# Optimization experiments

Hardware: AMD Instinct MI355X
Metric: run time of the kernel (lower is better)

The kernel has to match this reference:

```python
import jax, jax.numpy as jnp
import numpy as np

B, N, D = 4, 4096, 128
H = 128  # hidden_size == input_size (required by residual add)

def setup_inputs() -> dict:
    key = jax.random.key(0)
    kx, kw, kb = jax.random.split(key, 3)
    x = jax.random.normal(kx, (B, N, D), dtype=jnp.float32)
    # nn.Linear(input_size, hidden_size): weight [H, D], bias [H]
    lim = 1.0 / np.sqrt(D)
    W = jax.random.uniform(kw, (H, D), dtype=jnp.float32, minval=-lim, maxval=lim)
    b = jax.random.uniform(kb, (H,), dtype=jnp.float32, minval=-lim, maxval=lim)
    return {"x": x, "W": W, "b": b}

def reference(x, W, b):
    # adj[b,i,j] = <x[b,i], x[b,j]>, relu
    adj = jax.nn.relu(jnp.einsum('bid,bjd->bij', x, x))  # [B,N,N]
    # torch sums over dim=1 (rows) -> per-column sums, then divides columns
    col_sum = adj.sum(axis=1)                 # [B,N]
    adj = adj / col_sum[:, None, :]           # broadcast over dim 1
    out = jnp.einsum('bij,bjd->bid', adj, x)  # aggregate
    out = jnp.tanh(jnp.einsum('bnd,hd->bnh', out, W) + b)
    # Dropout(0.5) treated as eval-mode identity
    return out + x  # residual=True
```

## Files before the change

### kernel.cpp

```cpp
#include <hip/hip_runtime.h>
#include <hip/hip_bf16.h>

#define BN 4
#define NN 4096
#define DD 128

typedef __attribute__((ext_vector_type(8))) __bf16 bf16x8;
typedef __attribute__((ext_vector_type(4))) float f32x4;

typedef union {
  bf16x8 v;
  unsigned int u[4];
  uint2 u2[2];
} pk8;

typedef __attribute__((address_space(1))) const unsigned int* gas_p;
typedef __attribute__((address_space(3))) unsigned int* las_p;

__device__ __forceinline__ void gload16(const void* g, void* l) {
  __builtin_amdgcn_global_load_lds((gas_p)g, (las_p)l, 16, 0, 0);
}
__device__ __forceinline__ void wait_vm0() {
  asm volatile("s_waitcnt vmcnt(0)" ::: "memory");
}
__device__ __forceinline__ void wait_vm4() {
  asm volatile("s_waitcnt vmcnt(4)" ::: "memory");
}
__device__ __forceinline__ unsigned int cvtpk(float lo, float hi) {
  unsigned int r;
  asm("v_cvt_pk_bf16_f32 %0, %1, %2" : "=v"(r) : "v"(lo), "v"(hi));
  return r;
}
__device__ __forceinline__ unsigned int pkrelu(float lo, float hi) {
  return cvtpk(fmaxf(lo, 0.f), fmaxf(hi, 0.f));
}

__device__ inline unsigned short f2bf(float f) {
  unsigned int u = __float_as_uint(f);
  unsigned int r = (u + 0x7FFFu + ((u >> 16) & 1u)) >> 16;
  return (unsigned short)r;
}
__device__ inline float bf2f(unsigned short s) {
  return __uint_as_float(((unsigned int)s) << 16);
}

__global__ __launch_bounds__(256) void k_cvt(const float* __restrict__ x,
                                             unsigned short* __restrict__ xb) {
  int i = (blockIdx.x * 256 + threadIdx.x) * 8;
  float4 a = *(const float4*)(x + i);
  float4 c = *(const float4*)(x + i + 4);
  uint4 o;
  o.x = cvtpk(a.x, a.y);
  o.y = cvtpk(a.z, a.w);
  o.z = cvtpk(c.x, c.y);
  o.w = cvtpk(c.z, c.w);
  *(uint4*)(xb + i) = o;
}

__global__ __launch_bounds__(256, 4) void k_colsum(const unsigned short* __restrict__ xb,
                                                   float* __restrict__ colpart) {
  __shared__ unsigned short XiB[2][64 * 128];
  const int b = blockIdx.y, j0 = blockIdx.x * 128, ic = blockIdx.z;
  const int tid = threadIdx.x, lane = tid & 63, wv = tid >> 6;
  const unsigned short* xbb = xb + b * NN * DD;
  const int g = lane >> 4;
  const int ibeg = ic * (NN / 8);
  const int nt = (NN / 8) / 64;

#pragma unroll
  for (int hb = 0; hb < 2; ++hb)
#pragma unroll
    for (int q = 0; q < 4; ++q) {
      int c = wv * 4 + q;
      int lr = c * 4 + g;
      int gsrc = (lane & 15) ^ (lr & 7);
      gload16(&xbb[(j0 + hb * 64 + lr) * 128 + gsrc * 8], &XiB[hb][c * 512]);
    }
  wait_vm0();
  __syncthreads();

  bf16x8 bfr[2][4];
#pragma unroll
  for (int ni = 0; ni < 2; ++ni)
#pragma unroll
    for (int kk = 0; kk < 4; ++kk) {
      int lr = (wv & 1) * 32 + ni * 16 + (lane & 15);
      bfr[ni][kk] = *(const bf16x8*)&XiB[wv >> 1][lr * 128 + (((kk * 4 + g) ^ (lr & 7)) << 3)];
    }
  __syncthreads();

#pragma unroll
  for (int q = 0; q < 4; ++q) {
    int c = wv * 4 + q;
    int lr = c * 4 + g;
    int gsrc = (lane & 15) ^ (lr & 7);
    gload16(&xbb[(ibeg + lr) * 128 + gsrc * 8], &XiB[1][c * 512]);
  }

  int basek[4];
#pragma unroll
  for (int kk = 0; kk < 4; ++kk)
    basek[kk] = (lane & 15) * 128 + (((kk * 4 + g) ^ (lane & 7)) << 3);

  float colacc0 = 0.f, colacc1 = 0.f;
  for (int t = 0; t < nt; ++t) {
    wait_vm0();
    __syncthreads();
    const int cur = (t + 1) & 1, nxt = t & 1;
    if (t + 1 < nt) {
      const int i1 = ibeg + (t + 1) * 64;
#pragma unroll
      for (int q = 0; q < 4; ++q) {
        int c = wv * 4 + q;
        int lr = c * 4 + g;
        int gsrc = (lane & 15) ^ (lr & 7);
        gload16(&xbb[(i1 + lr) * 128 + gsrc * 8], &XiB[nxt][c * 512]);
      }
    }
    f32x4 a0[4], a1[4];
#pragma unroll
    for (int mj = 0; mj < 4; ++mj) { a0[mj] = (f32x4){}; a1[mj] = (f32x4){}; }
    __builtin_amdgcn_s_setprio(1);
#pragma unroll
    for (int kk = 0; kk < 4; ++kk) {
      bf16x8 ar0 = *(const bf16x8*)&XiB[cur][basek[kk]];
      bf16x8 ar1 = *(const bf16x8*)&XiB[cur][basek[kk] + 1 * 2048];
      bf16x8 ar2 = *(const bf16x8*)&XiB[cur][basek[kk] + 2 * 2048];
      bf16x8 ar3 = *(const bf16x8*)&XiB[cur][basek[kk] + 3 * 2048];
      a0[0] = __builtin_amdgcn_mfma_f32_16x16x32_bf16(ar0, bfr[0][kk], a0[0], 0, 0, 0);
      a1[0] = __builtin_amdgcn_mfma_f32_16x16x32_bf16(ar0, bfr[1][kk], a1[0], 0, 0, 0);
      a0[1] = __builtin_amdgcn_mfma_f32_16x16x32_bf16(ar1, bfr[0][kk], a0[1], 0, 0, 0);
      a1[1] = __builtin_amdgcn_mfma_f32_16x16x32_bf16(ar1, bfr[1][kk], a1[1], 0, 0, 0);
      a0[2] = __builtin_amdgcn_mfma_f32_16x16x32_bf16(ar2, bfr[0][kk], a0[2], 0, 0, 0);
      a1[2] = __builtin_amdgcn_mfma_f32_16x16x32_bf16(ar2, bfr[1][kk], a1[2], 0, 0, 0);
      a0[3] = __builtin_amdgcn_mfma_f32_16x16x32_bf16(ar3, bfr[0][kk], a0[3], 0, 0, 0);
      a1[3] = __builtin_amdgcn_mfma_f32_16x16x32_bf16(ar3, bfr[1][kk], a1[3], 0, 0, 0);
    }
    __builtin_amdgcn_s_setprio(0);
    {
      float s0 = 0.f, s1 = 0.f;
#pragma unroll
      for (int mj = 0; mj < 4; ++mj)
#pragma unroll
        for (int r = 0; r < 4; ++r) {
          s0 += fmaxf(a0[mj][r], 0.f);
          s1 += fmaxf(a1[mj][r], 0.f);
        }
      s0 += __shfl_xor(s0, 16); s0 += __shfl_xor(s0, 32);
      s1 += __shfl_xor(s1, 16); s1 += __shfl_xor(s1, 32);
      colacc0 += s0; colacc1 += s1;
    }
  }
  if (lane < 16) {
    colpart[(ic * BN + b) * NN + j0 + wv * 32 + lane] = colacc0;
    colpart[(ic * BN + b) * NN + j0 + wv * 32 + 16 + lane] = colacc1;
  }
}

__global__ __launch_bounds__(256) void k_ytrans(const float* __restrict__ x,
                                                const float* __restrict__ colpart,
                                                unsigned short* __restrict__ yt) {
  __shared__ unsigned short T[64 * 72];
  const int b = blockIdx.z, j0 = blockIdx.y * 64, d0 = blockIdx.x * 64;
  const int tid = threadIdx.x;
  int jr = tid >> 2, q0 = (tid & 3) * 16;
  float cs = 0.f;
#pragma unroll
  for (int ic = 0; ic < 8; ++ic) cs += colpart[(ic * BN + b) * NN + j0 + jr];
  float inv = 1.0f / cs;
  const float* xr = x + (size_t)(b * NN + j0 + jr) * DD + d0 + q0;
#pragma unroll
  for (int q = 0; q < 4; ++q) {
    float4 v = *(const float4*)(xr + q * 4);
    int dc = q0 + q * 4;
    T[jr * 72 + dc + 0] = f2bf(v.x * inv);
    T[jr * 72 + dc + 1] = f2bf(v.y * inv);
    T[jr * 72 + dc + 2] = f2bf(v.z * inv);
    T[jr * 72 + dc + 3] = f2bf(v.w * inv);
  }
  __syncthreads();
  for (int c = tid; c < 512; c += 256) {
    int dr = c >> 3, jg = c & 7;
    alignas(16) unsigned short tmp[8];
#pragma unroll
    for (int u = 0; u < 8; ++u) {
      int jj = (jg >> 2) * 32 + (jg & 3) * 4 + (u & 3) + (u >> 2) * 16;
      tmp[u] = T[jj * 72 + dr];
    }
    *(uint4*)&yt[(size_t)(b * DD + d0 + dr) * NN + j0 + jg * 8] = *(const uint4*)tmp;
  }
}

__global__ __launch_bounds__(256, 2) void k_pass2(const unsigned short* __restrict__ xb,
                                                  const unsigned short* __restrict__ yt,
                                                  unsigned short* __restrict__ opart,
                                                  int jc) {
  __shared__ unsigned short XjB[2][64 * 128];
  __shared__ unsigned short YsB[3][128 * 64];
  const int b = blockIdx.y, i0 = blockIdx.x * 128, zc = blockIdx.z;
  const int tid = threadIdx.x, lane = tid & 63, wv = tid >> 6;
  const unsigned short* xbb = xb + b * NN * DD;
  const unsigned short* ytb = yt + (size_t)b * DD * NN;
  const int g = lane >> 4, l15 = lane & 15;

  const int jspan = NN / jc;
  const int jbeg = zc * jspan;
  const int nt = jspan / 64;

#pragma unroll
  for (int hb = 0; hb < 2; ++hb)
#pragma unroll
    for (int q = 0; q < 4; ++q) {
      int c = wv * 4 + q;
      int lr = c * 4 + g;
      int gsrc = l15 ^ (lr & 7);
      gload16(&xbb[(i0 + hb * 64 + lr) * 128 + gsrc * 8], &XjB[hb][c * 512]);
    }
  wait_vm0();
  __syncthreads();

  bf16x8 bfr[2][4];
#pragma unroll
  for (int ni = 0; ni < 2; ++ni)
#pragma unroll
    for (int kk = 0; kk < 4; ++kk) {
      int lr = (wv & 1) * 32 + ni * 16 + l15;
      bfr[ni][kk] = *(const bf16x8*)&XjB[wv >> 1][lr * 128 + (((kk * 4 + g) ^ (lr & 7)) << 3)];
    }
  __syncthreads();

#pragma unroll
  for (int q = 0; q < 4; ++q) {
    int c = wv * 4 + q;
    int lr = c * 4 + g;
    int gsrc = l15 ^ (lr & 7);
    gload16(&xbb[(jbeg + lr) * 128 + gsrc * 8], &XjB[0][c * 512]);
  }
#pragma unroll
  for (int q = 0; q < 4; ++q) {
    int c = wv * 4 + q;
    int dr = c * 8 + (lane >> 3);
    int gsrc = (lane & 7) ^ (dr & 7);
    gload16(&ytb[(size_t)dr * NN + jbeg + gsrc * 8], &YsB[0][c * 512]);
  }
  if (1 < nt) {
#pragma unroll
    for (int q = 0; q < 4; ++q) {
      int c = wv * 4 + q;
      int dr = c * 8 + (lane >> 3);
      int gsrc = (lane & 7) ^ (dr & 7);
      gload16(&ytb[(size_t)dr * NN + jbeg + 64 + gsrc * 8], &YsB[1][c * 512]);
    }
  }

  int xjb[4];
#pragma unroll
  for (int kk = 0; kk < 4; ++kk)
    xjb[kk] = l15 * 128 + (((kk * 4 + g) ^ (l15 & 7)) << 3);
  int ysb[2];
#pragma unroll
  for (int c = 0; c < 2; ++c)
    ysb[c] = l15 * 64 + (((c * 4 + g) ^ (l15 & 7)) << 3);

  f32x4 oacc0[8], oacc1[8];
#pragma unroll
  for (int n = 0; n < 8; ++n) { oacc0[n] = (f32x4){}; oacc1[n] = (f32x4){}; }

  int ybuf = 0;
  for (int t = 0; t < nt; ++t) {
    if (t + 1 < nt) wait_vm4(); else wait_vm0();
    __syncthreads();
    if (t + 1 < nt) {
      const int j1 = jbeg + (t + 1) * 64;
#pragma unroll
      for (int q = 0; q < 4; ++q) {
        int c = wv * 4 + q;
        int lr = c * 4 + g;
        int gsrc = l15 ^ (lr & 7);
        gload16(&xbb[(j1 + lr) * 128 + gsrc * 8], &XjB[(t + 1) & 1][c * 512]);
      }
      if (t + 2 < nt) {
        const int j2 = jbeg + (t + 2) * 64;
        int nb = ybuf + 2; if (nb >= 3) nb -= 3;
#pragma unroll
        for (int q = 0; q < 4; ++q) {
          int c = wv * 4 + q;
          int dr = c * 8 + (lane >> 3);
          int gsrc = (lane & 7) ^ (dr & 7);
          gload16(&ytb[(size_t)dr * NN + j2 + gsrc * 8], &YsB[nb][c * 512]);
        }
      }
    }
    const unsigned short* Xj = XjB[t & 1];
    const unsigned short* Ys = YsB[ybuf];

    f32x4 s0[4], s1[4];
#pragma unroll
    for (int mj = 0; mj < 4; ++mj) { s0[mj] = (f32x4){}; s1[mj] = (f32x4){}; }
    __builtin_amdgcn_s_setprio(1);
#pragma unroll
    for (int kk = 0; kk < 4; ++kk) {
      bf16x8 ar0 = *(const bf16x8*)&Xj[xjb[kk]];
      bf16x8 ar1 = *(const bf16x8*)&Xj[xjb[kk] + 1 * 2048];
      bf16x8 ar2 = *(const bf16x8*)&Xj[xjb[kk] + 2 * 2048];
      bf16x8 ar3 = *(const bf16x8*)&Xj[xjb[kk] + 3 * 2048];
      s0[0] = __builtin_amdgcn_mfma_f32_16x16x32_bf16(ar0, bfr[0][kk], s0[0], 0, 0, 0);
      s1[0] = __builtin_amdgcn_mfma_f32_16x16x32_bf16(ar0, bfr[1][kk], s1[0], 0, 0, 0);
      s0[1] = __builtin_amdgcn_mfma_f32_16x16x32_bf16(ar1, bfr[0][kk], s0[1], 0, 0, 0);
      s1[1] = __builtin_amdgcn_mfma_f32_16x16x32_bf16(ar1, bfr[1][kk], s1[1], 0, 0, 0);
      s0[2] = __builtin_amdgcn_mfma_f32_16x16x32_bf16(ar2, bfr[0][kk], s0[2], 0, 0, 0);
      s1[2] = __builtin_amdgcn_mfma_f32_16x16x32_bf16(ar2, bfr[1][kk], s1[2], 0, 0, 0);
      s0[3] = __builtin_amdgcn_mfma_f32_16x16x32_bf16(ar3, bfr[0][kk], s0[3], 0, 0, 0);
      s1[3] = __builtin_amdgcn_mfma_f32_16x16x32_bf16(ar3, bfr[1][kk], s1[3], 0, 0, 0);
    }
    __builtin_amdgcn_s_setprio(0);
    pk8 p00, p01, p10, p11;
    p00.u[0] = pkrelu(s0[0][0], s0[0][1]); p00.u[1] = pkrelu(s0[0][2], s0[0][3]);
    p00.u[2] = pkrelu(s0[1][0], s0[1][1]); p00.u[3] = pkrelu(s0[1][2], s0[1][3]);
    p01.u[0] = pkrelu(s1[0][0], s1[0][1]); p01.u[1] = pkrelu(s1[0][2], s1[0][3]);
    p01.u[2] = pkrelu(s1[1][0], s1[1][1]); p01.u[3] = pkrelu(s1[1][2], s1[1][3]);
    p10.u[0] = pkrelu(s0[2][0], s0[2][1]); p10.u[1] = pkrelu(s0[2][2], s0[2][3]);
    p10.u[2] = pkrelu(s0[3][0], s0[3][1]); p10.u[3] = pkrelu(s0[3][2], s0[3][3]);
    p11.u[0] = pkrelu(s1[2][0], s1[2][1]); p11.u[1] = pkrelu(s1[2][2], s1[2][3]);
    p11.u[2] = pkrelu(s1[3][0], s1[3][1]); p11.u[3] = pkrelu(s1[3][2], s1[3][3]);
    __builtin_amdgcn_s_setprio(1);
#pragma unroll
    for (int n = 0; n < 8; ++n) {
      bf16x8 bb0 = *(const bf16x8*)&Ys[ysb[0] + n * 1024];
      bf16x8 bb1 = *(const bf16x8*)&Ys[ysb[1] + n * 1024];
      oacc0[n] = __builtin_amdgcn_mfma_f32_16x16x32_bf16(p00.v, bb0, oacc0[n], 0, 0, 0);
      oacc1[n] = __builtin_amdgcn_mfma_f32_16x16x32_bf16(p01.v, bb0, oacc1[n], 0, 0, 0);
      oacc0[n] = __builtin_amdgcn_mfma_f32_16x16x32_bf16(p10.v, bb1, oacc0[n], 0, 0, 0);
      oacc1[n] = __builtin_amdgcn_mfma_f32_16x16x32_bf16(p11.v, bb1, oacc1[n], 0, 0, 0);
    }
    __builtin_amdgcn_s_setprio(0);
    ++ybuf; if (ybuf == 3) ybuf = 0;
  }

  __syncthreads();
  unsigned short* sb = &XjB[0][0];
#pragma unroll
  for (int m = 0; m < 2; ++m)
#pragma unroll
    for (int n = 0; n < 8; ++n)
#pragma unroll
      for (int r = 0; r < 4; ++r) {
        int row = wv * 32 + m * 16 + g * 4 + r;
        int col = n * 16 + l15;
        sb[row * 128 + (((col >> 3) ^ (row & 7)) << 3) + (col & 7)] =
            f2bf(m == 0 ? oacc0[n][r] : oacc1[n][r]);
      }
  __syncthreads();
  for (int c = tid; c < 2048; c += 256) {
    int row = c >> 4, gq = c & 15;
    *(uint4*)&opart[((size_t)zc * (BN * NN) + b * NN + i0 + row) * DD + gq * 8] =
        *(const uint4*)&sb[row * 128 + ((gq ^ (row & 7)) << 3)];
  }
}

__global__ __launch_bounds__(256) void k_final(const unsigned short* __restrict__ opart,
                                               int jc,
                                               const float* __restrict__ W,
                                               const float* __restrict__ bias,
                                               const float* __restrict__ x,
                                               float* __restrict__ out) {
  __shared__ unsigned short Wb[128 * 128];
  __shared__ unsigned short PreS[32 * 128];
  const int tid = threadIdx.x, lane = tid & 63, wv = tid >> 6;
  const int g = lane >> 4;
  const int r0 = blockIdx.x * 32;

  {
    int h = tid >> 1, k0h = (tid & 1) * 8;
    const float* wr = W + h * 128 + k0h * 8;
#pragma unroll
    for (int q = 0; q < 8; ++q) {
      float4 v0 = *(const float4*)(wr + q * 8);
      float4 v1 = *(const float4*)(wr + q * 8 + 4);
      uint4 o;
      o.x = cvtpk(v0.x, v0.y); o.y = cvtpk(v0.z, v0.w);
      o.z = cvtpk(v1.x, v1.y); o.w = cvtpk(v1.z, v1.w);
      int gq = k0h + q;
      *(uint4*)&Wb[h * 128 + ((gq ^ (h & 7)) << 3)] = o;
    }
  }
  for (int c = tid; c < 512; c += 256) {
    int row = c >> 4, gq = c & 15;
    float s[8] = {0.f, 0.f, 0.f, 0.f, 0.f, 0.f, 0.f, 0.f};
    for (int ch = 0; ch < jc; ++ch) {
      uint4 pk = *(const uint4*)&opart[((size_t)ch * (BN * NN) + r0 + row) * DD + gq * 8];
      alignas(16) unsigned short us[8];
      *(uint4*)us = pk;
#pragma unroll
      for (int u = 0; u < 8; ++u) s[u] += bf2f(us[u]);
    }
    uint4 o;
    o.x = cvtpk(s[0], s[1]); o.y = cvtpk(s[2], s[3]);
    o.z = cvtpk(s[4], s[5]); o.w = cvtpk(s[6], s[7]);
    *(uint4*)&PreS[row * 128 + ((gq ^ (row & 7)) << 3)] = o;
  }
  __syncthreads();

  bf16x8 af[2][4], bf[2][4];
#pragma unroll
  for (int m = 0; m < 2; ++m)
#pragma unroll
    for (int kk = 0; kk < 4; ++kk) {
      int row = m * 16 + (lane & 15);
      af[m][kk] = *(const bf16x8*)&PreS[row * 128 + (((kk * 4 + g) ^ (row & 7)) << 3)];
    }
#pragma unroll
  for (int n = 0; n < 2; ++n)
#pragma unroll
    for (int kk = 0; kk < 4; ++kk) {
      int h = wv * 32 + n * 16 + (lane & 15);
      bf[n][kk] = *(const bf16x8*)&Wb[h * 128 + (((kk * 4 + g) ^ (h & 7)) << 3)];
    }

  f32x4 acc[2][2] = {};
#pragma unroll
  for (int kk = 0; kk < 4; ++kk) {
    acc[0][0] = __builtin_amdgcn_mfma_f32_16x16x32_bf16(af[0][kk], bf[0][kk], acc[0][0], 0, 0, 0);
    acc[0][1] = __builtin_amdgcn_mfma_f32_16x16x32_bf16(af[0][kk], bf[1][kk], acc[0][1], 0, 0, 0);
    acc[1][0] = __builtin_amdgcn_mfma_f32_16x16x32_bf16(af[1][kk], bf[0][kk], acc[1][0], 0, 0, 0);
    acc[1][1] = __builtin_amdgcn_mfma_f32_16x16x32_bf16(af[1][kk], bf[1][kk], acc[1][1], 0, 0, 0);
  }

  float bh0 = bias[wv * 32 + (lane & 15)];
  float bh1 = bias[wv * 32 + 16 + (lane & 15)];
#pragma unroll
  for (int m = 0; m < 2; ++m)
#pragma unroll
    for (int n = 0; n < 2; ++n)
#pragma unroll
      for (int r = 0; r < 4; ++r) {
        int row = r0 + m * 16 + g * 4 + r;
        int h = wv * 32 + n * 16 + (lane & 15);
        size_t idx = (size_t)row * 128 + h;
        out[idx] = tanhf(acc[m][n][r] + (n == 0 ? bh0 : bh1)) + x[idx];
      }
}

extern "C" void kernel_launch(void* const* d_in, const int* in_sizes, int n_in,
                              void* d_out, int out_size, void* d_ws, size_t ws_size,
                              hipStream_t stream) {
  (void)in_sizes; (void)n_in; (void)out_size;
  const float* x = (const float*)d_in[0];
  const float* W = (const float*)d_in[1];
  const float* bias = (const float*)d_in[2];
  float* out = (float*)d_out;
  char* ws = (char*)d_ws;
  unsigned short* xb = (unsigned short*)ws;
  unsigned short* yt = (unsigned short*)(ws + (4u << 20));
  float* colpart = (float*)(ws + (8u << 20));
  unsigned short* opart = (unsigned short*)(ws + (9u << 20));

  const size_t need4 = (9u << 20) + 4u * (4u << 20);
  const int jc = (ws_size >= need4) ? 4 : 1;

  k_cvt<<<1024, 256, 0, stream>>>(x, xb);
  k_colsum<<<dim3(32, 4, 8), 256, 0, stream>>>(xb, colpart);
  k_ytrans<<<dim3(2, 64, 4), 256, 0, stream>>>(x, colpart, yt);
  k_pass2<<<dim3(32, 4, jc), 256, 0, stream>>>(xb, yt, opart, jc);
  k_final<<<512, 256, 0, stream>>>(opart, jc, W, bias, x, out);
}
```

Measured before the change: 81.72 us.

## Software-pipeline score MFMA of next tile with aggregation MFMA of current tile

Restructures the main loop so the score GEMM for tile t+1 is issued before the aggregation GEMM for tile t. This lets the relu/pack dependency on S be hidden behind independent MFMA work. The X tile is now prefetched two tiles ahead alongside Y, with a prologue that computes the first score tile and waits with vmcnt(12). It keeps one extra set of score accumulators live across iterations, which raises register pressure, and changes the buffer reuse and wait counts in ways that must stay correct.

New measurement: 80.05 us, median of 2. 2.0% less time.

```diff
diff --git a/kernel.cpp b/kernel.cpp
--- a/kernel.cpp
+++ b/kernel.cpp
@@ -25,6 +25,9 @@
 }
 __device__ __forceinline__ void wait_vm4() {
   asm volatile("s_waitcnt vmcnt(4)" ::: "memory");
+}
+__device__ __forceinline__ void wait_vm12() {
+  asm volatile("s_waitcnt vmcnt(12)" ::: "memory");
 }
 __device__ __forceinline__ unsigned int cvtpk(float lo, float hi) {
   unsigned int r;
@@ -247,6 +250,13 @@
 #pragma unroll
     for (int q = 0; q < 4; ++q) {
       int c = wv * 4 + q;
+      int lr = c * 4 + g;
+      int gsrc = l15 ^ (lr & 7);
+      gload16(&xbb[(jbeg + 64 + lr) * 128 + gsrc * 8], &XjB[1][c * 512]);
+    }
+#pragma unroll
+    for (int q = 0; q < 4; ++q) {
+      int c = wv * 4 + q;
       int dr = c * 8 + (lane >> 3);
       int gsrc = (lane & 7) ^ (dr & 7);
       gload16(&ytb[(size_t)dr * NN + jbeg + 64 + gsrc * 8], &YsB[1][c * 512]);
@@ -266,37 +276,13 @@
 #pragma unroll
   for (int n = 0; n < 8; ++n) { oacc0[n] = (f32x4){}; oacc1[n] = (f32x4){}; }
 
-  int ybuf = 0;
-  for (int t = 0; t < nt; ++t) {
-    if (t + 1 < nt) wait_vm4(); else wait_vm0();
-    __syncthreads();
-    if (t + 1 < nt) {
-      const int j1 = jbeg + (t + 1) * 64;
-#pragma unroll
-      for (int q = 0; q < 4; ++q) {
-        int c = wv * 4 + q;
-        int lr = c * 4 + g;
-        int gsrc = l15 ^ (lr & 7);
-        gload16(&xbb[(j1 + lr) * 128 + gsrc * 8], &XjB[(t + 1) & 1][c * 512]);
-      }
-      if (t + 2 < nt) {
-        const int j2 = jbeg + (t + 2) * 64;
-        int nb = ybuf + 2; if (nb >= 3) nb -= 3;
-#pragma unroll
-        for (int q = 0; q < 4; ++q) {
-          int c = wv * 4 + q;
-          int dr = c * 8 + (lane >> 3);
-          int gsrc = (lane & 7) ^ (dr & 7);
-          gload16(&ytb[(size_t)dr * NN + j2 + gsrc * 8], &YsB[nb][c * 512]);
-        }
-      }
-    }
-    const unsigned short* Xj = XjB[t & 1];
-    const unsigned short* Ys = YsB[ybuf];
-
-    f32x4 s0[4], s1[4];
-#pragma unroll
-    for (int mj = 0; mj < 4; ++mj) { s0[mj] = (f32x4){}; s1[mj] = (f32x4){}; }
+  f32x4 s0[4], s1[4];
+#pragma unroll
+  for (int mj = 0; mj < 4; ++mj) { s0[mj] = (f32x4){}; s1[mj] = (f32x4){}; }
+  if (nt > 1) wait_vm12(); else wait_vm0();
+  __syncthreads();
+  {
+    const unsigned short* Xj = XjB[0];
     __builtin_amdgcn_s_setprio(1);
 #pragma unroll
     for (int kk = 0; kk < 4; ++kk) {
@@ -314,6 +300,30 @@
       s1[3] = __builtin_amdgcn_mfma_f32_16x16x32_bf16(ar3, bfr[1][kk], s1[3], 0, 0, 0);
     }
     __builtin_amdgcn_s_setprio(0);
+  }
+
+  int ybuf = 0;
+  for (int t = 0; t < nt; ++t) {
+    if (t + 1 < nt) wait_vm4(); else wait_vm0();
+    __syncthreads();
+    if (t + 2 < nt) {
+      const int j2 = jbeg + (t + 2) * 64;
+#pragma unroll
+      for (int q = 0; q < 4; ++q) {
+        int c = wv * 4 + q;
+        int lr = c * 4 + g;
+        int gsrc = l15 ^ (lr & 7);
+        gload16(&xbb[(j2 + lr) * 128 + gsrc * 8], &XjB[t & 1][c * 512]);
+      }
+      int nb = ybuf + 2; if (nb >= 3) nb -= 3;
+#pragma unroll
+      for (int q = 0; q < 4; ++q) {
+        int c = wv * 4 + q;
+        int dr = c * 8 + (lane >> 3);
+        int gsrc = (lane & 7) ^ (dr & 7);
+        gload16(&ytb[(size_t)dr * NN + j2 + gsrc * 8], &YsB[nb][c * 512]);
+      }
+    }
     pk8 p00, p01, p10, p11;
     p00.u[0] = pkrelu(s0[0][0], s0[0][1]); p00.u[1] = pkrelu(s0[0][2], s0[0][3]);
     p00.u[2] = pkrelu(s0[1][0], s0[1][1]); p00.u[3] = pkrelu(s0[1][2], s0[1][3]);
@@ -323,7 +333,29 @@
     p10.u[2] = pkrelu(s0[3][0], s0[3][1]); p10.u[3] = pkrelu(s0[3][2], s0[3][3]);
     p11.u[0] = pkrelu(s1[2][0], s1[2][1]); p11.u[1] = pkrelu(s1[2][2], s1[2][3]);
     p11.u[2] = pkrelu(s1[3][0], s1[3][1]); p11.u[3] = pkrelu(s1[3][2], s1[3][3]);
+
+    const unsigned short* Ys = YsB[ybuf];
     __builtin_amdgcn_s_setprio(1);
+    if (t + 1 < nt) {
+      const unsigned short* Xj = XjB[(t + 1) & 1];
+#pragma unroll
+      for (int mj = 0; mj < 4; ++mj) { s0[mj] = (f32x4){}; s1[mj] = (f32x4){}; }
+#pragma unroll
+      for (int kk = 0; kk < 4; ++kk) {
+        bf16x8 ar0 = *(const bf16x8*)&Xj[xjb[kk]];
+        bf16x8 ar1 = *(const bf16x8*)&Xj[xjb[kk] + 1 * 2048];
+        bf16x8 ar2 = *(const bf16x8*)&Xj[xjb[kk] + 2 * 2048];
+        bf16x8 ar3 = *(const bf16x8*)&Xj[xjb[kk] + 3 * 2048];
+        s0[0] = __builtin_amdgcn_mfma_f32_16x16x32_bf16(ar0, bfr[0][kk], s0[0], 0, 0, 0);
+        s1[0] = __builtin_amdgcn_mfma_f32_16x16x32_bf16(ar0, bfr[1][kk], s1[0], 0, 0, 0);
+        s0[1] = __builtin_amdgcn_mfma_f32_16x16x32_bf16(ar1, bfr[0][kk], s0[1], 0, 0, 0);
+        s1[1] = __builtin_amdgcn_mfma_f32_16x16x32_bf16(ar1, bfr[1][kk], s1[1], 0, 0, 0);
+        s0[2] = __builtin_amdgcn_mfma_f32_16x16x32_bf16(ar2, bfr[0][kk], s0[2], 0, 0, 0);
+        s1[2] = __builtin_amdgcn_mfma_f32_16x16x32_bf16(ar2, bfr[1][kk], s1[2], 0, 0, 0);
+        s0[3] = __builtin_amdgcn_mfma_f32_16x16x32_bf16(ar3, bfr[0][kk], s0[3], 0, 0, 0);
+        s1[3] = __builtin_amdgcn_mfma_f32_16x16x32_bf16(ar3, bfr[1][kk], s1[3], 0, 0, 0);
+      }
+    }
 #pragma unroll
     for (int n = 0; n < 8; ++n) {
       bf16x8 bb0 = *(const bf16x8*)&Ys[ysb[0] + n * 1024];
```
